# Optimization experiments

Hardware: AMD Instinct MI355X
Metric: run time of the kernel (lower is better)

The kernel has to match this reference:

```python
import jax, jax.numpy as jnp
import numpy as np

B, I, H = 32768, 128, 128


def setup_inputs() -> dict:
    key = jax.random.key(0)
    ks = jax.random.split(key, 11)
    s = 1.0 / np.sqrt(H)
    return {
        "x": jax.random.normal(ks[0], (B, I), jnp.float32),
        "h": jax.random.normal(ks[1], (B, H), jnp.float32),
        "c": jax.random.normal(ks[2], (B, H), jnp.float32),
        "W1": jax.random.normal(ks[3], (H, I + H), jnp.float32) * s,
        "b1": jax.random.normal(ks[4], (H,), jnp.float32) * s + 1.0,  # forget-gate bias offset 1.0
        "W2": jax.random.normal(ks[5], (H, I + H), jnp.float32) * s,
        "b2": jax.random.normal(ks[6], (H,), jnp.float32) * s,
        "Wf": jax.random.normal(ks[7], (H, I + H), jnp.float32) * s,
        "bf": jax.random.normal(ks[8], (H,), jnp.float32) * s,
        "W3": jax.random.normal(ks[9], (H, I + H), jnp.float32) * s,
        "b3": jax.random.normal(ks[10], (H,), jnp.float32) * s,
    }


def reference(x, h, c, W1, b1, W2, b2, Wf, bf, W3, b3):
    # total_in = inp + hidden (coordinate-list concat == feature concat)
    total = jnp.concatenate([x, h], axis=-1)  # [B, I+H]
    sig1 = jax.nn.sigmoid(total @ W1.T + b1)  # forget gate (bias offset +1)
    sig2 = jax.nn.sigmoid(total @ W2.T + b2)  # input gate
    f_l = jnp.tanh(total @ Wf.T + bf)         # candidate via symmetric f
    sig3 = jax.nn.sigmoid(total @ W3.T + b3)  # output gate
    new_c = c * sig1 + sig2 * f_l             # fused elementwise combine
    new_h = jnp.tanh(new_c) * sig3
    return new_h, new_c
```

## Files before the change

### kernel.cpp

```cpp
#include <hip/hip_runtime.h>

#define B_TOTAL 32768
#define NROWB   128
#define TILE    32
#define NT      4

typedef __attribute__((ext_vector_type(8)))  short    bf16x8;
typedef __attribute__((ext_vector_type(4)))  float    f32x4;
typedef __attribute__((ext_vector_type(4)))  unsigned u32x4;

__device__ __forceinline__ unsigned rne1(float f) {
    unsigned u = __builtin_bit_cast(unsigned, f);
    return (u + 0x7FFFu + ((u >> 16) & 1u)) >> 16;
}
__device__ __forceinline__ unsigned cvtpk(float lo, float hi) {
    unsigned r;
    asm("v_cvt_pk_bf16_f32 %0, %1, %2" : "=v"(r) : "v"(lo), "v"(hi));
    return r;
}
__device__ __forceinline__ float fsig(float v) {
    return __fdividef(1.0f, 1.0f + __expf(-v));
}
__device__ __forceinline__ float ftanh(float v) {
    return 1.0f - __fdividef(2.0f, 1.0f + __expf(2.0f * v));
}

__global__ void wconv_kernel(const float* __restrict__ w1, const float* __restrict__ w2,
                             const float* __restrict__ wf, const float* __restrict__ w3,
                             u32x4* __restrict__ out) {
    int T = blockIdx.x * 256 + threadIdx.x;
    int F = T >> 6, l = T & 63;
    int cs = F >> 5, g = (F >> 3) & 3, ks = F & 7;
    const float* W = (g == 0) ? w1 : (g == 1) ? w2 : (g == 2) ? wf : w3;
    const float* s = W + (cs * 16 + (l & 15)) * 256 + ks * 32 + (l >> 4) * 8;
    f32x4 lo = *(const f32x4*)s;
    f32x4 hi = *(const f32x4*)(s + 4);
    u32x4 r;
    r[0] = rne1(lo[0]) | (rne1(lo[1]) << 16);
    r[1] = rne1(lo[2]) | (rne1(lo[3]) << 16);
    r[2] = rne1(hi[0]) | (rne1(hi[1]) << 16);
    r[3] = rne1(hi[2]) | (rne1(hi[3]) << 16);
    out[T] = r;
}

__global__ __launch_bounds__(512, 2) void lstm_kernel(
    const float* __restrict__ x, const float* __restrict__ h, const float* __restrict__ c,
    const bf16x8* __restrict__ wfrag,
    const float* __restrict__ b1, const float* __restrict__ b2,
    const float* __restrict__ bfv, const float* __restrict__ b3,
    float* __restrict__ out)
{
    __shared__ __align__(16) char smem[2][TILE * 1024];

    const int tid  = threadIdx.x;
    const int wave = tid >> 6;
    const int lane = tid & 63;
    const int rb   = lane & 15;
    const int c4   = lane >> 4;
    const long row0 = (long)blockIdx.x * NROWB;
    const int gcol4 = wave * 16 + c4 * 4;

    auto STAGE = [&](int b, int tc) {
        char* buf = smem[b & 1];
        const long gr0 = row0 + (long)tc * TILE;
#pragma unroll
        for (int i = 0; i < 4; ++i) {
            const int r = wave * 4 + i;
            const unsigned kb = ((unsigned)lane * 16u) ^ (((unsigned)r & 7u) << 4);
            const float* src = (kb < 512u)
                ? (x + (gr0 + r) * 128 + (kb >> 2))
                : (h + (gr0 + r) * 128 + ((kb - 512u) >> 2));
            __builtin_amdgcn_global_load_lds(
                (const __attribute__((address_space(1))) unsigned*)src,
                (__attribute__((address_space(3))) unsigned*)(buf + r * 1024),
                16, 0, 0);
        }
    };

    STAGE(0, 0);

    bf16x8 wfr[4][8];
#pragma unroll
    for (int g = 0; g < 4; ++g)
#pragma unroll
        for (int ks = 0; ks < 8; ++ks)
            wfr[g][ks] = wfrag[(size_t)(wave * 32 + g * 8 + ks) * 64 + lane];

    f32x4 bias[4];
    bias[0] = *(const f32x4*)(b1 + gcol4);
    bias[1] = *(const f32x4*)(b2 + gcol4);
    bias[2] = *(const f32x4*)(bfv + gcol4);
    bias[3] = *(const f32x4*)(b3 + gcol4);

    f32x4 cv0 = *(const f32x4*)(c + (row0 + rb) * 128 + gcol4);
    f32x4 cv1 = *(const f32x4*)(c + (row0 + 16 + rb) * 128 + gcol4);

    float* out_h = out;
    float* out_c = out + (size_t)B_TOTAL * 128;

#pragma unroll 1
    for (int t = 0; t < NT; ++t) {
        asm volatile("s_waitcnt vmcnt(6)" ::: "memory");
        __builtin_amdgcn_s_barrier();
        __builtin_amdgcn_sched_barrier(0);

        const int tn = (t + 1 < NT) ? (t + 1) : (NT - 1);
        STAGE(t + 1, tn);
        f32x4 ncv0 = *(const f32x4*)(c + (row0 + (long)tn * TILE + rb) * 128 + gcol4);
        f32x4 ncv1 = *(const f32x4*)(c + (row0 + (long)tn * TILE + 16 + rb) * 128 + gcol4);

        const char* buf = smem[t & 1];
        const long gr0 = row0 + (long)t * TILE;

        f32x4 acc[2][4];
#pragma unroll
        for (int g = 0; g < 4; ++g) { acc[0][g] = bias[g]; acc[1][g] = bias[g]; }

#pragma unroll
        for (int ks = 0; ks < 8; ++ks) {
            bf16x8 af[2];
#pragma unroll
            for (int mt = 0; mt < 2; ++mt) {
                const int r = mt * 16 + rb;
                const unsigned swz = ((unsigned)r & 7u) << 4;
                const unsigned kb  = (unsigned)(ks * 128 + c4 * 32);
                const char* p = buf + r * 1024;
                f32x4 a0 = *(const f32x4*)(p + (kb ^ swz));
                f32x4 a1 = *(const f32x4*)(p + ((kb + 16u) ^ swz));
                union { unsigned u[4]; bf16x8 v; } pk;
                pk.u[0] = cvtpk(a0[0], a0[1]);
                pk.u[1] = cvtpk(a0[2], a0[3]);
                pk.u[2] = cvtpk(a1[0], a1[1]);
                pk.u[3] = cvtpk(a1[2], a1[3]);
                af[mt] = pk.v;
            }
#pragma unroll
            for (int g = 0; g < 4; ++g) {
                acc[0][g] = __builtin_amdgcn_mfma_f32_16x16x32_bf16(wfr[g][ks], af[0], acc[0][g], 0, 0, 0);
                acc[1][g] = __builtin_amdgcn_mfma_f32_16x16x32_bf16(wfr[g][ks], af[1], acc[1][g], 0, 0, 0);
            }
        }

#pragma unroll
        for (int mt = 0; mt < 2; ++mt) {
            const f32x4 cv = mt ? cv1 : cv0;
            f32x4 nh, nc;
#pragma unroll
            for (int j = 0; j < 4; ++j) {
                const float g1 = fsig(acc[mt][0][j]);
                const float g2 = fsig(acc[mt][1][j]);
                const float gf = ftanh(acc[mt][2][j]);
                const float g3 = fsig(acc[mt][3][j]);
                nc[j] = cv[j] * g1 + g2 * gf;
                nh[j] = ftanh(nc[j]) * g3;
            }
            const long o = (gr0 + mt * 16 + rb) * 128 + gcol4;
            *(f32x4*)(out_h + o) = nh;
            *(f32x4*)(out_c + o) = nc;
        }

        cv0 = ncv0;
        cv1 = ncv1;
    }
}

extern "C" void kernel_launch(void* const* d_in, const int* in_sizes, int n_in,
                              void* d_out, int out_size, void* d_ws, size_t ws_size,
                              hipStream_t stream) {
    (void)in_sizes; (void)n_in; (void)out_size; (void)ws_size;
    const float* x  = (const float*)d_in[0];
    const float* h  = (const float*)d_in[1];
    const float* c  = (const float*)d_in[2];
    const float* W1 = (const float*)d_in[3];
    const float* b1 = (const float*)d_in[4];
    const float* W2 = (const float*)d_in[5];
    const float* b2 = (const float*)d_in[6];
    const float* Wf = (const float*)d_in[7];
    const float* bf = (const float*)d_in[8];
    const float* W3 = (const float*)d_in[9];
    const float* b3 = (const float*)d_in[10];

    wconv_kernel<<<64, 256, 0, stream>>>(W1, W2, Wf, W3, (u32x4*)d_ws);
    lstm_kernel<<<B_TOTAL / NROWB, 512, 0, stream>>>(
        x, h, c, (const bf16x8*)d_ws, b1, b2, bf, b3, (float*)d_out);
}
```

Before: 35.09 us.

## Stage activations through registers as bf16 in LDS instead of direct fp32 global-to-LDS loads

Replaces the direct global_load_lds fp32 staging with register loads that are converted to bf16 once and written to LDS in an MFMA-friendly k-chunk-major layout. The MFMA loop then reads ready bf16 fragments, so each wave no longer repeats the fp32-to-bf16 conversion and LDS traffic is halved. Global prefetch runs two tiles ahead in registers, and the LDS store of the next tile is done after the MFMAs. In exchange it adds register pressure and a VGPR round trip, and it changes the wait from vmcnt to lgkmcnt.

```diff
diff --git a/kernel.cpp b/kernel.cpp
--- a/kernel.cpp
+++ b/kernel.cpp
@@ -50,7 +50,7 @@
     const float* __restrict__ bfv, const float* __restrict__ b3,
     float* __restrict__ out)
 {
-    __shared__ __align__(16) char smem[2][TILE * 1024];
+    __shared__ __align__(16) char smem[2][16384];
 
     const int tid  = threadIdx.x;
     const int wave = tid >> 6;
@@ -60,24 +60,35 @@
     const long row0 = (long)blockIdx.x * NROWB;
     const int gcol4 = wave * 16 + c4 * 4;
 
-    auto STAGE = [&](int b, int tc) {
-        char* buf = smem[b & 1];
-        const long gr0 = row0 + (long)tc * TILE;
-#pragma unroll
-        for (int i = 0; i < 4; ++i) {
-            const int r = wave * 4 + i;
-            const unsigned kb = ((unsigned)lane * 16u) ^ (((unsigned)r & 7u) << 4);
-            const float* src = (kb < 512u)
-                ? (x + (gr0 + r) * 128 + (kb >> 2))
-                : (h + (gr0 + r) * 128 + ((kb - 512u) >> 2));
-            __builtin_amdgcn_global_load_lds(
-                (const __attribute__((address_space(1))) unsigned*)src,
-                (__attribute__((address_space(3))) unsigned*)(buf + r * 1024),
-                16, 0, 0);
-        }
+    const int srow   = wave * 4 + (lane >> 4);
+    const int kchunk = lane & 15;
+
+    f32x4 ar[4];
+    auto A_ISSUE = [&](int t) {
+        const float* base = (kchunk < 8)
+            ? (x + (row0 + (long)t * TILE + srow) * 128 + kchunk * 16)
+            : (h + (row0 + (long)t * TILE + srow) * 128 + (kchunk - 8) * 16);
+        ar[0] = *(const f32x4*)(base);
+        ar[1] = *(const f32x4*)(base + 4);
+        ar[2] = *(const f32x4*)(base + 8);
+        ar[3] = *(const f32x4*)(base + 12);
+    };
+    auto A_STORE = [&](int b) {
+        u32x4 w0, w1;
+        w0[0] = cvtpk(ar[0][0], ar[0][1]);
+        w0[1] = cvtpk(ar[0][2], ar[0][3]);
+        w0[2] = cvtpk(ar[1][0], ar[1][1]);
+        w0[3] = cvtpk(ar[1][2], ar[1][3]);
+        w1[0] = cvtpk(ar[2][0], ar[2][1]);
+        w1[1] = cvtpk(ar[2][2], ar[2][3]);
+        w1[2] = cvtpk(ar[3][0], ar[3][1]);
+        w1[3] = cvtpk(ar[3][2], ar[3][3]);
+        char* dst = smem[b & 1] + (kchunk >> 1) * 2048 + srow * 64 + (kchunk & 1) * 32;
+        *(u32x4*)(dst)      = w0;
+        *(u32x4*)(dst + 16) = w1;
     };
 
-    STAGE(0, 0);
+    A_ISSUE(0);
 
     bf16x8 wfr[4][8];
 #pragma unroll
@@ -92,6 +103,9 @@
     bias[2] = *(const f32x4*)(bfv + gcol4);
     bias[3] = *(const f32x4*)(b3 + gcol4);
 
+    A_STORE(0);
+    A_ISSUE(1);
+
     f32x4 cv0 = *(const f32x4*)(c + (row0 + rb) * 128 + gcol4);
     f32x4 cv1 = *(const f32x4*)(c + (row0 + 16 + rb) * 128 + gcol4);
 
@@ -100,14 +114,9 @@
 
 #pragma unroll 1
     for (int t = 0; t < NT; ++t) {
-        asm volatile("s_waitcnt vmcnt(6)" ::: "memory");
+        asm volatile("s_waitcnt lgkmcnt(0)" ::: "memory");
         __builtin_amdgcn_s_barrier();
         __builtin_amdgcn_sched_barrier(0);
-
-        const int tn = (t + 1 < NT) ? (t + 1) : (NT - 1);
-        STAGE(t + 1, tn);
-        f32x4 ncv0 = *(const f32x4*)(c + (row0 + (long)tn * TILE + rb) * 128 + gcol4);
-        f32x4 ncv1 = *(const f32x4*)(c + (row0 + (long)tn * TILE + 16 + rb) * 128 + gcol4);
 
         const char* buf = smem[t & 1];
         const long gr0 = row0 + (long)t * TILE;
@@ -118,27 +127,24 @@
 
 #pragma unroll
         for (int ks = 0; ks < 8; ++ks) {
-            bf16x8 af[2];
-#pragma unroll
-            for (int mt = 0; mt < 2; ++mt) {
-                const int r = mt * 16 + rb;
-                const unsigned swz = ((unsigned)r & 7u) << 4;
-                const unsigned kb  = (unsigned)(ks * 128 + c4 * 32);
-                const char* p = buf + r * 1024;
-                f32x4 a0 = *(const f32x4*)(p + (kb ^ swz));
-                f32x4 a1 = *(const f32x4*)(p + ((kb + 16u) ^ swz));
-                union { unsigned u[4]; bf16x8 v; } pk;
-                pk.u[0] = cvtpk(a0[0], a0[1]);
-                pk.u[1] = cvtpk(a0[2], a0[3]);
-                pk.u[2] = cvtpk(a1[0], a1[1]);
-                pk.u[3] = cvtpk(a1[2], a1[3]);
-                af[mt] = pk.v;
-            }
+            bf16x8 af0 = *(const bf16x8*)(buf + ks * 2048 + rb * 64 + c4 * 16);
+            bf16x8 af1 = *(const bf16x8*)(buf + ks * 2048 + (16 + rb) * 64 + c4 * 16);
 #pragma unroll
             for (int g = 0; g < 4; ++g) {
-                acc[0][g] = __builtin_amdgcn_mfma_f32_16x16x32_bf16(wfr[g][ks], af[0], acc[0][g], 0, 0, 0);
-                acc[1][g] = __builtin_amdgcn_mfma_f32_16x16x32_bf16(wfr[g][ks], af[1], acc[1][g], 0, 0, 0);
+                acc[0][g] = __builtin_amdgcn_mfma_f32_16x16x32_bf16(wfr[g][ks], af0, acc[0][g], 0, 0, 0);
+                acc[1][g] = __builtin_amdgcn_mfma_f32_16x16x32_bf16(wfr[g][ks], af1, acc[1][g], 0, 0, 0);
             }
+        }
+
+        if (t + 1 < NT) {
+            A_STORE(t + 1);
+            if (t + 2 < NT) A_ISSUE(t + 2);
+        }
+
+        f32x4 ncv0, ncv1;
+        if (t + 1 < NT) {
+            ncv0 = *(const f32x4*)(c + (gr0 + TILE + rb) * 128 + gcol4);
+            ncv1 = *(const f32x4*)(c + (gr0 + TILE + 16 + rb) * 128 + gcol4);
         }
 
 #pragma unroll
@@ -159,8 +165,7 @@
             *(f32x4*)(out_c + o) = nc;
         }
 
-        cv0 = ncv0;
-        cv1 = ncv1;
+        if (t + 1 < NT) { cv0 = ncv0; cv1 = ncv1; }
     }
 }
 
```

Result: faster. 32.41 us, median of 3 (-7.6%).
